# Kernel tuning notes

Hardware: AMD Instinct MI355X
Metric: run time of the kernel (lower is better)

## Reference

```python
import jax, jax.numpy as jnp
import numpy as np

B, S, D = 4, 2048, 1024  # batch, seq_len, input_dimension
KD, VD = 1024, 1024      # key_dim, value_dim


def setup_inputs() -> dict:
    key = jax.random.key(0)
    ks = jax.random.split(key, 9)
    sc_in = 1.0 / np.sqrt(D)
    sc_v = 1.0 / np.sqrt(VD)
    return {
        "x":  jax.random.normal(ks[0], (B, S, D), dtype=jnp.float32),
        "Wq": jax.random.normal(ks[1], (KD, D), dtype=jnp.float32) * sc_in,
        "bq": jax.random.normal(ks[2], (KD,), dtype=jnp.float32) * 0.01,
        "Wk": jax.random.normal(ks[3], (KD, D), dtype=jnp.float32) * sc_in,
        "bk": jax.random.normal(ks[4], (KD,), dtype=jnp.float32) * 0.01,
        "Wv": jax.random.normal(ks[5], (VD, D), dtype=jnp.float32) * sc_in,
        "bv": jax.random.normal(ks[6], (VD,), dtype=jnp.float32) * 0.01,
        "Wo": jax.random.normal(ks[7], (D, VD), dtype=jnp.float32) * sc_v,
        "bo": jax.random.normal(ks[8], (D,), dtype=jnp.float32) * 0.01,
    }


def reference(x, Wq, bq, Wk, bk, Wv, bv, Wo, bo):
    # projections (torch Linear: x @ W.T + b)
    q = jnp.einsum('bsd,kd->bsk', x, Wq) + bq   # (B,S,KD)
    k = jnp.einsum('bsd,kd->bsk', x, Wk) + bk   # (B,S,KD)
    v = jnp.einsum('bsd,vd->bsv', x, Wv) + bv   # (B,S,VD)

    scores = jnp.einsum('bqk,bsk->bqs', q, k) / jnp.sqrt(jnp.float32(KD))  # (B,S,S)

    # sign rescale: scores * sign(scores) (sign(0) mapped to 1) == |scores| with zeros kept
    sign_mask = jnp.sign(scores)
    sign_mask = sign_mask + (sign_mask == 0).astype(jnp.float32)

    # causal mask: lower-triangular (incl diag) multiplied by 1, strict upper -> -inf
    seq = scores.shape[-1]
    causal = jnp.tril(jnp.ones((seq, seq), dtype=bool))
    masked = jnp.where(causal, scores * sign_mask, -jnp.inf)

    weights = jax.nn.softmax(masked, axis=2)            # (B,S,S)
    out = jnp.einsum('bqs,bsv->bqv', weights, v)        # (B,S,VD)
    return jnp.einsum('bqv,dv->bqd', out, Wo) + bo      # (B,S,D)
```

## Files before the change

### kernel.cpp

```cpp
#include <hip/hip_runtime.h>
#include <hip/hip_bf16.h>
#include <cstdint>


#define BM 128

typedef __attribute__((ext_vector_type(8))) __bf16 bf16x8;
typedef __attribute__((ext_vector_type(4))) __bf16 bf16x4;
typedef __attribute__((ext_vector_type(4))) float floatx4;

__device__ __forceinline__ void async_copy16(const __bf16* g, const __bf16* l) {
  __builtin_amdgcn_global_load_lds(
      (const __attribute__((address_space(1))) unsigned int*)(const void*)g,
      (__attribute__((address_space(3))) unsigned int*)(unsigned)(uintptr_t)(const void*)l,
      16, 0, 0);
}

__device__ __forceinline__ void gemm_core(const __bf16* __restrict__ pA,
                                          const __bf16* __restrict__ pB,
                                          int K, int kBeg, int kEnd, int mb,
                                          int nb, floatx4 (&acc)[4][4]) {
  __shared__ __align__(16) __bf16 As0[BM * 32];
  __shared__ __align__(16) __bf16 As1[BM * 32];
  __shared__ __align__(16) __bf16 Bs0[BM * 32];
  __shared__ __align__(16) __bf16 Bs1[BM * 32];

  const int t = threadIdx.x;
  const int lane = t & 63;
  const int wave = t >> 6;
  const int quad = lane >> 4;
  const int l16 = lane & 15;
  const int wm = wave >> 1;
  const int wn = wave & 1;

  const __bf16* gA = pA + (long)(mb * BM + (t >> 2)) * K + ((t & 3) * 8);
  const __bf16* gB = pB + (long)(nb * BM + (t >> 2)) * K + ((t & 3) * 8);
  const long rowHalf = (long)64 * K;
  __bf16* lA0 = &As0[t * 8];
  __bf16* lA1 = &As1[t * 8];
  __bf16* lB0 = &Bs0[t * 8];
  __bf16* lB1 = &Bs1[t * 8];

  for (int kk = kBeg; kk < kEnd; ++kk) {
    const long ko = (long)kk * 64;
    async_copy16(gA + ko, lA0);
    async_copy16(gA + ko + rowHalf, lA0 + 2048);
    async_copy16(gA + ko + 32, lA1);
    async_copy16(gA + ko + 32 + rowHalf, lA1 + 2048);
    async_copy16(gB + ko, lB0);
    async_copy16(gB + ko + rowHalf, lB0 + 2048);
    async_copy16(gB + ko + 32, lB1);
    async_copy16(gB + ko + 32 + rowHalf, lB1 + 2048);
    __syncthreads();

#pragma unroll
    for (int p = 0; p < 2; ++p) {
      const __bf16* As = p ? As1 : As0;
      const __bf16* Bs = p ? Bs1 : Bs0;
      bf16x8 af[4], bfr[4];
#pragma unroll
      for (int i = 0; i < 4; ++i) {
        af[i] = *(const bf16x8*)&As[(wm * 64 + i * 16 + l16) * 32 + quad * 8];
        bfr[i] = *(const bf16x8*)&Bs[(wn * 64 + i * 16 + l16) * 32 + quad * 8];
      }
#pragma unroll
      for (int i = 0; i < 4; ++i)
#pragma unroll
        for (int j = 0; j < 4; ++j)
          acc[i][j] = __builtin_amdgcn_mfma_f32_16x16x32_bf16(af[i], bfr[j],
                                                              acc[i][j], 0, 0, 0);
    }
    __syncthreads();
  }
}

__device__ __forceinline__ float wave_sum(float s) {
  s += __shfl_xor(s, 1, 64);
  s += __shfl_xor(s, 2, 64);
  s += __shfl_xor(s, 4, 64);
  s += __shfl_xor(s, 8, 64);
  s += __shfl_xor(s, 16, 64);
  s += __shfl_xor(s, 32, 64);
  return s;
}

__global__ void __launch_bounds__(256, 2)
wcomb(const __bf16* __restrict__ Wqt, const __bf16* __restrict__ Wkt,
      const __bf16* __restrict__ Wob, const __bf16* __restrict__ Wvt,
      __bf16* __restrict__ Mqk, __bf16* __restrict__ Wvo,
      const float* __restrict__ bq, const float* __restrict__ bk,
      float* __restrict__ w1, float* __restrict__ w2, float* __restrict__ cbuf) {
  const int id = blockIdx.x;
  const int t = threadIdx.x;

  if (id < 128) {
    const bool isM = id < 64;
    const int wid = isM ? id : (id - 64);
    const int mb = wid >> 3, nb = wid & 7;
    const __bf16* pA = isM ? Wkt : Wob;
    const __bf16* pB = isM ? Wqt : Wvt;
    __bf16* C = isM ? Mqk : Wvo;

    floatx4 acc[4][4] = {};
    gemm_core(pA, pB, 1024, 0, 16, mb, nb, acc);

    const int lane = t & 63, wave = t >> 6;
    const int rb = (wave >> 1) * 64 + (lane >> 4) * 4;
    const int cb = (wave & 1) * 64 + (lane & 15);
#pragma unroll
    for (int j4 = 0; j4 < 4; ++j4) {
      const int gc = nb * 128 + cb + j4 * 16;
#pragma unroll
      for (int i = 0; i < 4; ++i) {
        const int gr = mb * BM + rb + i * 16;
#pragma unroll
        for (int r = 0; r < 4; ++r)
          C[(long)(gr + r) * 1024 + gc] = (__bf16)acc[i][j4][r];
      }
    }
  } else if (id < 144) {
    const bool is1 = id < 136;
    const int jb = is1 ? (id - 128) : (id - 136);
    const __bf16* Wt = is1 ? Wqt : Wkt;
    const float* bb = is1 ? bk : bq;
    float* ow = is1 ? w1 : w2;
    const int lane = t & 63, wave = t >> 6;
    for (int rr = 0; rr < 32; ++rr) {
      const int row = jb * 128 + wave * 32 + rr;
      const bf16x8 a0 = *(const bf16x8*)&Wt[(long)row * 1024 + lane * 16];
      const bf16x8 a1 = *(const bf16x8*)&Wt[(long)row * 1024 + lane * 16 + 8];
      float s = 0.f;
#pragma unroll
      for (int e = 0; e < 8; ++e) {
        s += (float)a0[e] * bb[lane * 16 + e];
        s += (float)a1[e] * bb[lane * 16 + 8 + e];
      }
      s = wave_sum(s);
      if (lane == 0) ow[row] = s;
    }
  } else {
    __shared__ float wsum[4];
    float s = 0.f;
    for (int i = t; i < 1024; i += 256) s += bq[i] * bk[i];
    s = wave_sum(s);
    if ((t & 63) == 0) wsum[t >> 6] = s;
    __syncthreads();
    if (t == 0) cbuf[0] = wsum[0] + wsum[1] + wsum[2] + wsum[3];
  }
}

__global__ void __launch_bounds__(256, 2)
proj(const __bf16* __restrict__ xb, const __bf16* __restrict__ Mqk,
     const __bf16* __restrict__ Wvo, const float* __restrict__ w2,
     const float* __restrict__ bvo, const float* __restrict__ w1,
     const float* __restrict__ cbuf, __bf16* __restrict__ yb,
     __bf16* __restrict__ Ut, float* __restrict__ r1, int S, int D) {
  const int id = blockIdx.x;
  const int t = threadIdx.x;

  if (id < 1024) {
    const bool isY = id < 512;
    const int pid = isY ? id : (id - 512);
    const int xcd = pid & 7;
    const int j = pid >> 3;
    const int mb = xcd * 8 + (j & 7);
    const int nb = j >> 3;
    const __bf16* pB = isY ? Mqk : Wvo;

    floatx4 acc[4][4] = {};
    gemm_core(xb, pB, D, 0, D / 64, mb, nb, acc);

    const int lane = t & 63, wave = t >> 6;
    const int rb = (wave >> 1) * 64 + (lane >> 4) * 4;
    const int cb = (wave & 1) * 64 + (lane & 15);

    if (isY) {
#pragma unroll
      for (int j4 = 0; j4 < 4; ++j4) {
        const int gc = nb * 128 + cb + j4 * 16;
        const float bv = w2[gc];
#pragma unroll
        for (int i = 0; i < 4; ++i) {
          const int gr = mb * BM + rb + i * 16;
#pragma unroll
          for (int r = 0; r < 4; ++r)
            yb[(long)(gr + r) * D + gc] = (__bf16)(acc[i][j4][r] + bv);
        }
      }
    } else {
      const int bb = (mb * BM) / S;
      const int s0 = mb * BM - bb * S;
#pragma unroll
      for (int j4 = 0; j4 < 4; ++j4) {
        const int gc = nb * 128 + cb + j4 * 16;
        const float bv = bvo[gc];
#pragma unroll
        for (int i = 0; i < 4; ++i) {
          const int sr = s0 + rb + i * 16;
          bf16x4 o;
#pragma unroll
          for (int r = 0; r < 4; ++r) o[r] = (__bf16)(acc[i][j4][r] + bv);
          *(bf16x4*)&Ut[((long)bb * D + gc) * S + sr] = o;
        }
      }
    }
  } else {
    const int jb = id - 1024;
    const float c = cbuf[0];
    const int lane = t & 63, wave = t >> 6;
    for (int rr = 0; rr < 32; ++rr) {
      const int row = jb * 128 + wave * 32 + rr;
      const bf16x8 a0 = *(const bf16x8*)&xb[(long)row * D + lane * 16];
      const bf16x8 a1 = *(const bf16x8*)&xb[(long)row * D + lane * 16 + 8];
      float s = 0.f;
#pragma unroll
      for (int e = 0; e < 8; ++e) {
        s += (float)a0[e] * w1[lane * 16 + e];
        s += (float)a1[e] * w1[lane * 16 + 8 + e];
      }
      s = wave_sum(s);
      if (lane == 0) r1[row] = s + c;
    }
  }
}

__global__ void __launch_bounds__(256, 2)
gemm_scores(const __bf16* __restrict__ yb, const __bf16* __restrict__ xb,
            const float* __restrict__ r1, __bf16* __restrict__ P,
            float* __restrict__ lsum, int S, int D) {
  const int id = blockIdx.x;
  const int xcd = id & 7;
  const int r = id >> 3;
  const int b = r / 17;
  const int ci = r - b * 17;
  const int n1 = xcd + 1;
  const int mb = (ci < n1) ? xcd : (15 - xcd);
  const int nb = (ci < n1) ? ci : (ci - n1);

  floatx4 acc[4][4] = {};
  gemm_core(yb + (long)b * S * D, xb + (long)b * S * D, D, 0, D / 64, mb, nb,
            acc);

  const int t = threadIdx.x;
  const int lane = t & 63, wave = t >> 6;
  const int l16 = lane & 15;
  const int rb = (wave >> 1) * 64 + (lane >> 4) * 4;
  const int cb = (wave & 1) * 64 + l16;
  __bf16* C = P + (long)b * S * S;
  float* lrow = lsum + (long)b * S;
  const float* r1b = r1 + (long)b * S;
  const float sc = 0.03125f;

#pragma unroll
  for (int i = 0; i < 4; ++i) {
#pragma unroll
    for (int r_ = 0; r_ < 4; ++r_) {
      const int row = mb * BM + rb + i * 16 + r_;
      const float rv = r1b[row];
      float psum = 0.f;
#pragma unroll
      for (int j4 = 0; j4 < 4; ++j4) {
        const int col = nb * 128 + cb + j4 * 16;
        const float p =
            (col <= row) ? __expf(fabsf((acc[i][j4][r_] + rv) * sc)) : 0.f;
        psum += p;
        C[(long)row * S + col] = (__bf16)p;
      }
      psum += __shfl_xor(psum, 1, 64);
      psum += __shfl_xor(psum, 2, 64);
      psum += __shfl_xor(psum, 4, 64);
      psum += __shfl_xor(psum, 8, 64);
      if (l16 == 0) atomicAdd(&lrow[row], psum);
    }
  }
}

__global__ void __launch_bounds__(256, 2)
gemm_pvo(const __bf16* __restrict__ P, const __bf16* __restrict__ Ut,
         const float* __restrict__ lsum, const float* __restrict__ bo,
         float* __restrict__ out, int S, int D) {
  const int id = blockIdx.x;
  const int xcd = id & 7;
  const int j = id >> 3;
  const int half = j >> 5;
  const int idx = j & 31;
  const int b = idx >> 3;
  const int nb = idx & 7;
  const int mb = half ? xcd : (15 - xcd);

  floatx4 acc[4][4] = {};
  gemm_core(P + (long)b * S * S, Ut + (long)b * D * S, S, 0, 2 * (mb + 1), mb,
            nb, acc);

  const int t = threadIdx.x;
  const int lane = t & 63, wave = t >> 6;
  const int rb = (wave >> 1) * 64 + (lane >> 4) * 4;
  const int cb = (wave & 1) * 64 + (lane & 15);
  const float* lrow = lsum + (long)b * S;

#pragma unroll
  for (int i = 0; i < 4; ++i) {
#pragma unroll
    for (int r_ = 0; r_ < 4; ++r_) {
      const int row = mb * BM + rb + i * 16 + r_;
      const float inv = 1.f / lrow[row];
#pragma unroll
      for (int j4 = 0; j4 < 4; ++j4) {
        const int col = nb * 128 + cb + j4 * 16;
        out[((long)b * S + row) * D + col] = acc[i][j4][r_] * inv + bo[col];
      }
    }
  }
}

__global__ void prep(const float* __restrict__ x, const float* __restrict__ Wq,
                     const float* __restrict__ Wk, const float* __restrict__ Wv,
                     const float* __restrict__ Wo, const float* __restrict__ bv,
                     __bf16* __restrict__ xb, __bf16* __restrict__ Wqt,
                     __bf16* __restrict__ Wkt, __bf16* __restrict__ Wvt,
                     __bf16* __restrict__ Wob, float* __restrict__ bvo,
                     float* __restrict__ lsum) {
  __shared__ __bf16 tile[64][66];
  __shared__ float wsum[4];
  const int bid = blockIdx.x;
  const int t = threadIdx.x;
  if (bid < 8192) {
    const long i = ((long)bid * 256 + t) * 4;
    const float4 f = *(const float4*)(x + i);
    bf16x4 o;
    o[0] = (__bf16)f.x; o[1] = (__bf16)f.y; o[2] = (__bf16)f.z; o[3] = (__bf16)f.w;
    *(bf16x4*)(xb + i) = o;
  } else if (bid < 8960) {
    const int which = (bid - 8192) >> 8;
    const int idx = (bid - 8192) & 255;
    const float* src = which == 0 ? Wq : (which == 1 ? Wk : Wv);
    __bf16* dst = which == 0 ? Wqt : (which == 1 ? Wkt : Wvt);
    const int r0 = (idx >> 4) * 64, c0 = (idx & 15) * 64;
#pragma unroll
    for (int e = 0; e < 16; ++e) {
      const int i = e * 256 + t;
      const int r = i >> 6, c = i & 63;
      tile[r][c] = (__bf16)src[(long)(r0 + r) * 1024 + (c0 + c)];
    }
    __syncthreads();
#pragma unroll
    for (int e = 0; e < 16; ++e) {
      const int i = e * 256 + t;
      const int r = i >> 6, c = i & 63;
      dst[(long)(c0 + r) * 1024 + (r0 + c)] = tile[c][r];
    }
  } else if (bid < 9984) {
    const long i = ((long)(bid - 8960) * 256 + t) * 4;
    const float4 f = *(const float4*)(Wo + i);
    bf16x4 o;
    o[0] = (__bf16)f.x; o[1] = (__bf16)f.y; o[2] = (__bf16)f.z; o[3] = (__bf16)f.w;
    *(bf16x4*)(Wob + i) = o;
  } else if (bid < 11008) {
    const int d = bid - 9984;
    const float* row = Wo + (long)d * 1024;
    float s = 0.f;
    for (int v = t; v < 1024; v += 256) s += bv[v] * row[v];
#pragma unroll
    for (int off = 32; off > 0; off >>= 1) s += __shfl_down(s, off, 64);
    if ((t & 63) == 0) wsum[t >> 6] = s;
    __syncthreads();
    if (t == 0) bvo[d] = wsum[0] + wsum[1] + wsum[2] + wsum[3];
  } else {
#pragma unroll
    for (int e = 0; e < 8; ++e)
      *(float4*)(lsum + (e * 256 + t) * 4) = float4{0.f, 0.f, 0.f, 0.f};
  }
}

extern "C" void kernel_launch(void* const* d_in, const int* in_sizes, int n_in,
                              void* d_out, int out_size, void* d_ws, size_t ws_size,
                              hipStream_t stream) {
  const float* x = (const float*)d_in[0];
  const float* Wq = (const float*)d_in[1];
  const float* bq = (const float*)d_in[2];
  const float* Wk = (const float*)d_in[3];
  const float* bk = (const float*)d_in[4];
  const float* Wv = (const float*)d_in[5];
  const float* bv = (const float*)d_in[6];
  const float* Wo = (const float*)d_in[7];
  const float* bo = (const float*)d_in[8];
  float* out = (float*)d_out;

  constexpr int B = 4, S = 2048, D = 1024;
  constexpr long MB_ = 1024 * 1024;

  char* w = (char*)d_ws;
  __bf16* xb  = (__bf16*)(w);
  __bf16* yb  = (__bf16*)(w + 16 * MB_);
  __bf16* Ut  = (__bf16*)(w + 32 * MB_);
  __bf16* P   = (__bf16*)(w + 48 * MB_);
  __bf16* Mqk = (__bf16*)(w + 80 * MB_);
  __bf16* Wvo = (__bf16*)(w + 82 * MB_);
  __bf16* Wqt = (__bf16*)(w + 84 * MB_);
  __bf16* Wkt = (__bf16*)(w + 86 * MB_);
  __bf16* Wvt = (__bf16*)(w + 88 * MB_);
  __bf16* Wob = (__bf16*)(w + 90 * MB_);
  float* lsum = (float*)(w + 92 * MB_);
  float* r1   = (float*)(w + 92 * MB_ + 32768);
  float* w1   = (float*)(w + 92 * MB_ + 65536);
  float* w2   = (float*)(w + 92 * MB_ + 69632);
  float* bvo  = (float*)(w + 92 * MB_ + 73728);
  float* cbuf = (float*)(w + 92 * MB_ + 77824);

  prep<<<11009, 256, 0, stream>>>(x, Wq, Wk, Wv, Wo, bv, xb, Wqt, Wkt, Wvt,
                                  Wob, bvo, lsum);

  wcomb<<<145, 256, 0, stream>>>(Wqt, Wkt, Wob, Wvt, Mqk, Wvo, bq, bk, w1, w2,
                                 cbuf);

  proj<<<1088, 256, 0, stream>>>(xb, Mqk, Wvo, w2, bvo, w1, cbuf, yb, Ut, r1,
                                 S, D);

  gemm_scores<<<544, 256, 0, stream>>>(yb, xb, r1, P, lsum, S, D);

  gemm_pvo<<<512, 256, 0, stream>>>(P, Ut, lsum, bo, out, S, D);
}
```

Before: 253.5 us.

## Fuse all five kernels into one persistent cooperative kernel with grid syncs

Replaces the five separate launches (prep, wcomb, proj, gemm_scores, gemm_pvo) with a single cooperative persistent kernel. Blocks loop over each stage's work items and a grid-wide sync separates the stages, all sharing one shared-memory buffer. The bias-projection reductions (w1, w2, bvo) are also rewritten to read the fp32 weights directly instead of the transposed bf16 copies. The aim is to cut launch gaps and tail effects between stages. In exchange it adds grid-sync cost, and the block-to-XCD mapping is no longer tied to blockIdx when the grid is smaller than the work count.

```diff
diff --git a/kernel.cpp b/kernel.cpp
--- a/kernel.cpp
+++ b/kernel.cpp
@@ -1,6 +1,9 @@
 #include <hip/hip_runtime.h>
+#include <hip/hip_cooperative_groups.h>
 #include <hip/hip_bf16.h>
 #include <cstdint>
+
+namespace cg = cooperative_groups;
 
 
 #define BM 128
@@ -8,6 +11,13 @@
 typedef __attribute__((ext_vector_type(8))) __bf16 bf16x8;
 typedef __attribute__((ext_vector_type(4))) __bf16 bf16x4;
 typedef __attribute__((ext_vector_type(4))) float floatx4;
+
+struct KArgs {
+  const float *x, *Wq, *bq, *Wk, *bk, *Wv, *bv, *Wo, *bo;
+  float* out;
+  __bf16 *xb, *yb, *Ut, *P, *Mqk, *Wvo, *Wqt, *Wkt, *Wvt, *Wob;
+  float *lsum, *r1, *w1, *w2, *bvo, *cbuf;
+};
 
 __device__ __forceinline__ void async_copy16(const __bf16* g, const __bf16* l) {
   __builtin_amdgcn_global_load_lds(
@@ -16,14 +26,14 @@
       16, 0, 0);
 }
 
-__device__ __forceinline__ void gemm_core(const __bf16* __restrict__ pA,
+__device__ __forceinline__ void gemm_core(__bf16* SM, const __bf16* __restrict__ pA,
                                           const __bf16* __restrict__ pB,
                                           int K, int kBeg, int kEnd, int mb,
                                           int nb, floatx4 (&acc)[4][4]) {
-  __shared__ __align__(16) __bf16 As0[BM * 32];
-  __shared__ __align__(16) __bf16 As1[BM * 32];
-  __shared__ __align__(16) __bf16 Bs0[BM * 32];
-  __shared__ __align__(16) __bf16 Bs1[BM * 32];
+  __bf16* As0 = SM;
+  __bf16* As1 = SM + 4096;
+  __bf16* Bs0 = SM + 8192;
+  __bf16* Bs1 = SM + 12288;
 
   const int t = threadIdx.x;
   const int lane = t & 63;
@@ -84,26 +94,102 @@
   return s;
 }
 
-__global__ void __launch_bounds__(256, 2)
-wcomb(const __bf16* __restrict__ Wqt, const __bf16* __restrict__ Wkt,
-      const __bf16* __restrict__ Wob, const __bf16* __restrict__ Wvt,
-      __bf16* __restrict__ Mqk, __bf16* __restrict__ Wvo,
-      const float* __restrict__ bq, const float* __restrict__ bk,
-      float* __restrict__ w1, float* __restrict__ w2, float* __restrict__ cbuf) {
-  const int id = blockIdx.x;
+__global__ void __launch_bounds__(256, 2) coop(KArgs a) {
+  __shared__ __align__(16) __bf16 SM[16384];
   const int t = threadIdx.x;
-
-  if (id < 128) {
-    const bool isM = id < 64;
-    const int wid = isM ? id : (id - 64);
+  const int gsz = gridDim.x;
+  cg::grid_group grid = cg::this_grid();
+  constexpr int S = 2048, D = 1024;
+
+  for (int bid = blockIdx.x; bid < 10010; bid += gsz) {
+    if (bid < 8192) {
+      const long i = ((long)bid * 256 + t) * 4;
+      const float4 f = *(const float4*)(a.x + i);
+      bf16x4 o;
+      o[0] = (__bf16)f.x; o[1] = (__bf16)f.y; o[2] = (__bf16)f.z; o[3] = (__bf16)f.w;
+      *(bf16x4*)(a.xb + i) = o;
+    } else if (bid < 8960) {
+      const int which = (bid - 8192) >> 8;
+      const int idx = (bid - 8192) & 255;
+      const float* src = which == 0 ? a.Wq : (which == 1 ? a.Wk : a.Wv);
+      __bf16* dst = which == 0 ? a.Wqt : (which == 1 ? a.Wkt : a.Wvt);
+      const int r0 = (idx >> 4) * 64, c0 = (idx & 15) * 64;
+      __bf16(*tile)[66] = reinterpret_cast<__bf16(*)[66]>(SM);
+      __syncthreads();
+#pragma unroll
+      for (int e = 0; e < 16; ++e) {
+        const int i = e * 256 + t;
+        const int r = i >> 6, c = i & 63;
+        tile[r][c] = (__bf16)src[(long)(r0 + r) * 1024 + (c0 + c)];
+      }
+      __syncthreads();
+#pragma unroll
+      for (int e = 0; e < 16; ++e) {
+        const int i = e * 256 + t;
+        const int r = i >> 6, c = i & 63;
+        dst[(long)(c0 + r) * 1024 + (r0 + c)] = tile[c][r];
+      }
+      __syncthreads();
+    } else if (bid < 9984) {
+      const long i = ((long)(bid - 8960) * 256 + t) * 4;
+      const float4 f = *(const float4*)(a.Wo + i);
+      bf16x4 o;
+      o[0] = (__bf16)f.x; o[1] = (__bf16)f.y; o[2] = (__bf16)f.z; o[3] = (__bf16)f.w;
+      *(bf16x4*)(a.Wob + i) = o;
+    } else if (bid < 9992) {
+      const int lane = t & 63, wave = t >> 6;
+      for (int rr = 0; rr < 32; ++rr) {
+        const int row = (bid - 9984) * 128 + wave * 32 + rr;
+        float s = 0.f;
+        for (int v = lane; v < 1024; v += 64) s += a.bv[v] * a.Wo[(long)row * 1024 + v];
+        s = wave_sum(s);
+        if (lane == 0) a.bvo[row] = s;
+      }
+    } else if (bid < 10008) {
+      const bool is1 = bid < 10000;
+      const int jb = is1 ? (bid - 9992) : (bid - 10000);
+      const float* W = is1 ? a.Wq : a.Wk;
+      const float* bb = is1 ? a.bk : a.bq;
+      float* ow = is1 ? a.w1 : a.w2;
+      const int d = jb * 128 + (t & 127);
+      const int half = t >> 7;
+      float s = 0.f;
+      for (int kd = half * 512; kd < half * 512 + 512; ++kd)
+        s += W[(long)kd * 1024 + d] * bb[kd];
+      float* fbuf = (float*)SM;
+      __syncthreads();
+      fbuf[t] = s;
+      __syncthreads();
+      if (t < 128) ow[jb * 128 + t] = fbuf[t] + fbuf[t + 128];
+      __syncthreads();
+    } else if (bid == 10008) {
+      float s = 0.f;
+      for (int i = t; i < 1024; i += 256) s += a.bq[i] * a.bk[i];
+      s = wave_sum(s);
+      float* fbuf = (float*)SM;
+      __syncthreads();
+      if ((t & 63) == 0) fbuf[t >> 6] = s;
+      __syncthreads();
+      if (t == 0) a.cbuf[0] = fbuf[0] + fbuf[1] + fbuf[2] + fbuf[3];
+      __syncthreads();
+    } else {
+#pragma unroll
+      for (int e = 0; e < 8; ++e)
+        *(float4*)(a.lsum + (e * 256 + t) * 4) = float4{0.f, 0.f, 0.f, 0.f};
+    }
+  }
+  __threadfence();
+  grid.sync();
+
+  for (int j = blockIdx.x; j < 128; j += gsz) {
+    const bool isM = j < 64;
+    const int wid = isM ? j : (j - 64);
     const int mb = wid >> 3, nb = wid & 7;
-    const __bf16* pA = isM ? Wkt : Wob;
-    const __bf16* pB = isM ? Wqt : Wvt;
-    __bf16* C = isM ? Mqk : Wvo;
-
+    const __bf16* pA = isM ? a.Wkt : a.Wob;
+    const __bf16* pB = isM ? a.Wqt : a.Wvt;
+    __bf16* C = isM ? a.Mqk : a.Wvo;
     floatx4 acc[4][4] = {};
-    gemm_core(pA, pB, 1024, 0, 16, mb, nb, acc);
-
+    gemm_core(SM, pA, pB, 1024, 0, 16, mb, nb, acc);
     const int lane = t & 63, wave = t >> 6;
     const int rb = (wave >> 1) * 64 + (lane >> 4) * 4;
     const int cb = (wave & 1) * 64 + (lane & 15);
@@ -118,305 +204,195 @@
           C[(long)(gr + r) * 1024 + gc] = (__bf16)acc[i][j4][r];
       }
     }
-  } else if (id < 144) {
-    const bool is1 = id < 136;
-    const int jb = is1 ? (id - 128) : (id - 136);
-    const __bf16* Wt = is1 ? Wqt : Wkt;
-    const float* bb = is1 ? bk : bq;
-    float* ow = is1 ? w1 : w2;
+  }
+  __threadfence();
+  grid.sync();
+
+  for (int j = blockIdx.x; j < 1088; j += gsz) {
+    if (j < 1024) {
+      const bool isY = j < 512;
+      const int pid = isY ? j : (j - 512);
+      const int xcd = pid & 7;
+      const int jj = pid >> 3;
+      const int mb = xcd * 8 + (jj & 7);
+      const int nb = jj >> 3;
+      const __bf16* pB = isY ? a.Mqk : a.Wvo;
+      floatx4 acc[4][4] = {};
+      gemm_core(SM, a.xb, pB, D, 0, D / 64, mb, nb, acc);
+      const int lane = t & 63, wave = t >> 6;
+      const int rb = (wave >> 1) * 64 + (lane >> 4) * 4;
+      const int cb = (wave & 1) * 64 + (lane & 15);
+      if (isY) {
+#pragma unroll
+        for (int j4 = 0; j4 < 4; ++j4) {
+          const int gc = nb * 128 + cb + j4 * 16;
+          const float bv = a.w2[gc];
+#pragma unroll
+          for (int i = 0; i < 4; ++i) {
+            const int gr = mb * BM + rb + i * 16;
+#pragma unroll
+            for (int r = 0; r < 4; ++r)
+              a.yb[(long)(gr + r) * D + gc] = (__bf16)(acc[i][j4][r] + bv);
+          }
+        }
+      } else {
+        const int bb = (mb * BM) / S;
+        const int s0 = mb * BM - bb * S;
+#pragma unroll
+        for (int j4 = 0; j4 < 4; ++j4) {
+          const int gc = nb * 128 + cb + j4 * 16;
+          const float bv = a.bvo[gc];
+#pragma unroll
+          for (int i = 0; i < 4; ++i) {
+            const int sr = s0 + rb + i * 16;
+            bf16x4 o;
+#pragma unroll
+            for (int r = 0; r < 4; ++r) o[r] = (__bf16)(acc[i][j4][r] + bv);
+            *(bf16x4*)&a.Ut[((long)bb * D + gc) * S + sr] = o;
+          }
+        }
+      }
+    } else {
+      const int jb = j - 1024;
+      const float c = a.cbuf[0];
+      const int lane = t & 63, wave = t >> 6;
+      for (int rr = 0; rr < 32; ++rr) {
+        const int row = jb * 128 + wave * 32 + rr;
+        const bf16x8 a0 = *(const bf16x8*)&a.xb[(long)row * D + lane * 16];
+        const bf16x8 a1 = *(const bf16x8*)&a.xb[(long)row * D + lane * 16 + 8];
+        float s = 0.f;
+#pragma unroll
+        for (int e = 0; e < 8; ++e) {
+          s += (float)a0[e] * a.w1[lane * 16 + e];
+          s += (float)a1[e] * a.w1[lane * 16 + 8 + e];
+        }
+        s = wave_sum(s);
+        if (lane == 0) a.r1[row] = s + c;
+      }
+    }
+  }
+  __threadfence();
+  grid.sync();
+
+  for (int j = blockIdx.x; j < 544; j += gsz) {
+    const int xcd = j & 7;
+    const int r = j >> 3;
+    const int b = r / 17;
+    const int ci = r - b * 17;
+    const int n1 = xcd + 1;
+    const int mb = (ci < n1) ? xcd : (15 - xcd);
+    const int nb = (ci < n1) ? ci : (ci - n1);
+    floatx4 acc[4][4] = {};
+    gemm_core(SM, a.yb + (long)b * S * D, a.xb + (long)b * S * D, D, 0, D / 64,
+              mb, nb, acc);
     const int lane = t & 63, wave = t >> 6;
-    for (int rr = 0; rr < 32; ++rr) {
-      const int row = jb * 128 + wave * 32 + rr;
-      const bf16x8 a0 = *(const bf16x8*)&Wt[(long)row * 1024 + lane * 16];
-      const bf16x8 a1 = *(const bf16x8*)&Wt[(long)row * 1024 + lane * 16 + 8];
-      float s = 0.f;
-#pragma unroll
-      for (int e = 0; e < 8; ++e) {
-        s += (float)a0[e] * bb[lane * 16 + e];
-        s += (float)a1[e] * bb[lane * 16 + 8 + e];
-      }
-      s = wave_sum(s);
-      if (lane == 0) ow[row] = s;
-    }
-  } else {
-    __shared__ float wsum[4];
-    float s = 0.f;
-    for (int i = t; i < 1024; i += 256) s += bq[i] * bk[i];
-    s = wave_sum(s);
-    if ((t & 63) == 0) wsum[t >> 6] = s;
-    __syncthreads();
-    if (t == 0) cbuf[0] = wsum[0] + wsum[1] + wsum[2] + wsum[3];
-  }
-}
-
-__global__ void __launch_bounds__(256, 2)
-proj(const __bf16* __restrict__ xb, const __bf16* __restrict__ Mqk,
-     const __bf16* __restrict__ Wvo, const float* __restrict__ w2,
-     const float* __restrict__ bvo, const float* __restrict__ w1,
-     const float* __restrict__ cbuf, __bf16* __restrict__ yb,
-     __bf16* __restrict__ Ut, float* __restrict__ r1, int S, int D) {
-  const int id = blockIdx.x;
-  const int t = threadIdx.x;
-
-  if (id < 1024) {
-    const bool isY = id < 512;
-    const int pid = isY ? id : (id - 512);
-    const int xcd = pid & 7;
-    const int j = pid >> 3;
-    const int mb = xcd * 8 + (j & 7);
-    const int nb = j >> 3;
-    const __bf16* pB = isY ? Mqk : Wvo;
-
+    const int l16 = lane & 15;
+    const int rb = (wave >> 1) * 64 + (lane >> 4) * 4;
+    const int cb = (wave & 1) * 64 + l16;
+    __bf16* C = a.P + (long)b * S * S;
+    float* lrow = a.lsum + (long)b * S;
+    const float* r1b = a.r1 + (long)b * S;
+    const float sc = 0.03125f;
+#pragma unroll
+    for (int i = 0; i < 4; ++i) {
+#pragma unroll
+      for (int r_ = 0; r_ < 4; ++r_) {
+        const int row = mb * BM + rb + i * 16 + r_;
+        const float rv = r1b[row];
+        float psum = 0.f;
+#pragma unroll
+        for (int j4 = 0; j4 < 4; ++j4) {
+          const int col = nb * 128 + cb + j4 * 16;
+          const float p =
+              (col <= row) ? __expf(fabsf((acc[i][j4][r_] + rv) * sc)) : 0.f;
+          psum += p;
+          C[(long)row * S + col] = (__bf16)p;
+        }
+        psum += __shfl_xor(psum, 1, 64);
+        psum += __shfl_xor(psum, 2, 64);
+        psum += __shfl_xor(psum, 4, 64);
+        psum += __shfl_xor(psum, 8, 64);
+        if (l16 == 0) atomicAdd(&lrow[row], psum);
+      }
+    }
+  }
+  __threadfence();
+  grid.sync();
+
+  for (int j = blockIdx.x; j < 512; j += gsz) {
+    const int xcd = j & 7;
+    const int jj = j >> 3;
+    const int half = jj >> 5;
+    const int idx = jj & 31;
+    const int b = idx >> 3;
+    const int nb = idx & 7;
+    const int mb = half ? xcd : (15 - xcd);
     floatx4 acc[4][4] = {};
-    gemm_core(xb, pB, D, 0, D / 64, mb, nb, acc);
-
+    gemm_core(SM, a.P + (long)b * S * S, a.Ut + (long)b * D * S, S, 0,
+              2 * (mb + 1), mb, nb, acc);
     const int lane = t & 63, wave = t >> 6;
     const int rb = (wave >> 1) * 64 + (lane >> 4) * 4;
     const int cb = (wave & 1) * 64 + (lane & 15);
-
-    if (isY) {
-#pragma unroll
-      for (int j4 = 0; j4 < 4; ++j4) {
-        const int gc = nb * 128 + cb + j4 * 16;
-        const float bv = w2[gc];
-#pragma unroll
-        for (int i = 0; i < 4; ++i) {
-          const int gr = mb * BM + rb + i * 16;
-#pragma unroll
-          for (int r = 0; r < 4; ++r)
-            yb[(long)(gr + r) * D + gc] = (__bf16)(acc[i][j4][r] + bv);
-        }
-      }
-    } else {
-      const int bb = (mb * BM) / S;
-      const int s0 = mb * BM - bb * S;
-#pragma unroll
-      for (int j4 = 0; j4 < 4; ++j4) {
-        const int gc = nb * 128 + cb + j4 * 16;
-        const float bv = bvo[gc];
-#pragma unroll
-        for (int i = 0; i < 4; ++i) {
-          const int sr = s0 + rb + i * 16;
-          bf16x4 o;
-#pragma unroll
-          for (int r = 0; r < 4; ++r) o[r] = (__bf16)(acc[i][j4][r] + bv);
-          *(bf16x4*)&Ut[((long)bb * D + gc) * S + sr] = o;
-        }
-      }
-    }
-  } else {
-    const int jb = id - 1024;
-    const float c = cbuf[0];
-    const int lane = t & 63, wave = t >> 6;
-    for (int rr = 0; rr < 32; ++rr) {
-      const int row = jb * 128 + wave * 32 + rr;
-      const bf16x8 a0 = *(const bf16x8*)&xb[(long)row * D + lane * 16];
-      const bf16x8 a1 = *(const bf16x8*)&xb[(long)row * D + lane * 16 + 8];
-      float s = 0.f;
-#pragma unroll
-      for (int e = 0; e < 8; ++e) {
-        s += (float)a0[e] * w1[lane * 16 + e];
-        s += (float)a1[e] * w1[lane * 16 + 8 + e];
-      }
-      s = wave_sum(s);
-      if (lane == 0) r1[row] = s + c;
-    }
-  }
-}
-
-__global__ void __launch_bounds__(256, 2)
-gemm_scores(const __bf16* __restrict__ yb, const __bf16* __restrict__ xb,
-            const float* __restrict__ r1, __bf16* __restrict__ P,
-            float* __restrict__ lsum, int S, int D) {
-  const int id = blockIdx.x;
-  const int xcd = id & 7;
-  const int r = id >> 3;
-  const int b = r / 17;
-  const int ci = r - b * 17;
-  const int n1 = xcd + 1;
-  const int mb = (ci < n1) ? xcd : (15 - xcd);
-  const int nb = (ci < n1) ? ci : (ci - n1);
-
-  floatx4 acc[4][4] = {};
-  gemm_core(yb + (long)b * S * D, xb + (long)b * S * D, D, 0, D / 64, mb, nb,
-            acc);
-
-  const int t = threadIdx.x;
-  const int lane = t & 63, wave = t >> 6;
-  const int l16 = lane & 15;
-  const int rb = (wave >> 1) * 64 + (lane >> 4) * 4;
-  const int cb = (wave & 1) * 64 + l16;
-  __bf16* C = P + (long)b * S * S;
-  float* lrow = lsum + (long)b * S;
-  const float* r1b = r1 + (long)b * S;
-  const float sc = 0.03125f;
-
-#pragma unroll
-  for (int i = 0; i < 4; ++i) {
-#pragma unroll
-    for (int r_ = 0; r_ < 4; ++r_) {
-      const int row = mb * BM + rb + i * 16 + r_;
-      const float rv = r1b[row];
-      float psum = 0.f;
-#pragma unroll
-      for (int j4 = 0; j4 < 4; ++j4) {
-        const int col = nb * 128 + cb + j4 * 16;
-        const float p =
-            (col <= row) ? __expf(fabsf((acc[i][j4][r_] + rv) * sc)) : 0.f;
-        psum += p;
-        C[(long)row * S + col] = (__bf16)p;
-      }
-      psum += __shfl_xor(psum, 1, 64);
-      psum += __shfl_xor(psum, 2, 64);
-      psum += __shfl_xor(psum, 4, 64);
-      psum += __shfl_xor(psum, 8, 64);
-      if (l16 == 0) atomicAdd(&lrow[row], psum);
-    }
-  }
-}
-
-__global__ void __launch_bounds__(256, 2)
-gemm_pvo(const __bf16* __restrict__ P, const __bf16* __restrict__ Ut,
-         const float* __restrict__ lsum, const float* __restrict__ bo,
-         float* __restrict__ out, int S, int D) {
-  const int id = blockIdx.x;
-  const int xcd = id & 7;
-  const int j = id >> 3;
-  const int half = j >> 5;
-  const int idx = j & 31;
-  const int b = idx >> 3;
-  const int nb = idx & 7;
-  const int mb = half ? xcd : (15 - xcd);
-
-  floatx4 acc[4][4] = {};
-  gemm_core(P + (long)b * S * S, Ut + (long)b * D * S, S, 0, 2 * (mb + 1), mb,
-            nb, acc);
-
-  const int t = threadIdx.x;
-  const int lane = t & 63, wave = t >> 6;
-  const int rb = (wave >> 1) * 64 + (lane >> 4) * 4;
-  const int cb = (wave & 1) * 64 + (lane & 15);
-  const float* lrow = lsum + (long)b * S;
-
-#pragma unroll
-  for (int i = 0; i < 4; ++i) {
-#pragma unroll
-    for (int r_ = 0; r_ < 4; ++r_) {
-      const int row = mb * BM + rb + i * 16 + r_;
-      const float inv = 1.f / lrow[row];
-#pragma unroll
-      for (int j4 = 0; j4 < 4; ++j4) {
-        const int col = nb * 128 + cb + j4 * 16;
-        out[((long)b * S + row) * D + col] = acc[i][j4][r_] * inv + bo[col];
-      }
-    }
-  }
-}
-
-__global__ void prep(const float* __restrict__ x, const float* __restrict__ Wq,
-                     const float* __restrict__ Wk, const float* __restrict__ Wv,
-                     const float* __restrict__ Wo, const float* __restrict__ bv,
-                     __bf16* __restrict__ xb, __bf16* __restrict__ Wqt,
-                     __bf16* __restrict__ Wkt, __bf16* __restrict__ Wvt,
-                     __bf16* __restrict__ Wob, float* __restrict__ bvo,
-                     float* __restrict__ lsum) {
-  __shared__ __bf16 tile[64][66];
-  __shared__ float wsum[4];
-  const int bid = blockIdx.x;
-  const int t = threadIdx.x;
-  if (bid < 8192) {
-    const long i = ((long)bid * 256 + t) * 4;
-    const float4 f = *(const float4*)(x + i);
-    bf16x4 o;
-    o[0] = (__bf16)f.x; o[1] = (__bf16)f.y; o[2] = (__bf16)f.z; o[3] = (__bf16)f.w;
-    *(bf16x4*)(xb + i) = o;
-  } else if (bid < 8960) {
-    const int which = (bid - 8192) >> 8;
-    const int idx = (bid - 8192) & 255;
-    const float* src = which == 0 ? Wq : (which == 1 ? Wk : Wv);
-    __bf16* dst = which == 0 ? Wqt : (which == 1 ? Wkt : Wvt);
-    const int r0 = (idx >> 4) * 64, c0 = (idx & 15) * 64;
-#pragma unroll
-    for (int e = 0; e < 16; ++e) {
-      const int i = e * 256 + t;
-      const int r = i >> 6, c = i & 63;
-      tile[r][c] = (__bf16)src[(long)(r0 + r) * 1024 + (c0 + c)];
-    }
-    __syncthreads();
-#pragma unroll
-    for (int e = 0; e < 16; ++e) {
-      const int i = e * 256 + t;
-      const int r = i >> 6, c = i & 63;
-      dst[(long)(c0 + r) * 1024 + (r0 + c)] = tile[c][r];
-    }
-  } else if (bid < 9984) {
-    const long i = ((long)(bid - 8960) * 256 + t) * 4;
-    const float4 f = *(const float4*)(Wo + i);
-    bf16x4 o;
-    o[0] = (__bf16)f.x; o[1] = (__bf16)f.y; o[2] = (__bf16)f.z; o[3] = (__bf16)f.w;
-    *(bf16x4*)(Wob + i) = o;
-  } else if (bid < 11008) {
-    const int d = bid - 9984;
-    const float* row = Wo + (long)d * 1024;
-    float s = 0.f;
-    for (int v = t; v < 1024; v += 256) s += bv[v] * row[v];
-#pragma unroll
-    for (int off = 32; off > 0; off >>= 1) s += __shfl_down(s, off, 64);
-    if ((t & 63) == 0) wsum[t >> 6] = s;
-    __syncthreads();
-    if (t == 0) bvo[d] = wsum[0] + wsum[1] + wsum[2] + wsum[3];
-  } else {
-#pragma unroll
-    for (int e = 0; e < 8; ++e)
-      *(float4*)(lsum + (e * 256 + t) * 4) = float4{0.f, 0.f, 0.f, 0.f};
+    const float* lrow = a.lsum + (long)b * S;
+#pragma unroll
+    for (int i = 0; i < 4; ++i) {
+#pragma unroll
+      for (int r_ = 0; r_ < 4; ++r_) {
+        const int row = mb * BM + rb + i * 16 + r_;
+        const float inv = 1.f / lrow[row];
+#pragma unroll
+        for (int j4 = 0; j4 < 4; ++j4) {
+          const int col = nb * 128 + cb + j4 * 16;
+          a.out[((long)b * S + row) * D + col] = acc[i][j4][r_] * inv + a.bo[col];
+        }
+      }
+    }
   }
 }
 
 extern "C" void kernel_launch(void* const* d_in, const int* in_sizes, int n_in,
                               void* d_out, int out_size, void* d_ws, size_t ws_size,
                               hipStream_t stream) {
-  const float* x = (const float*)d_in[0];
-  const float* Wq = (const float*)d_in[1];
-  const float* bq = (const float*)d_in[2];
-  const float* Wk = (const float*)d_in[3];
-  const float* bk = (const float*)d_in[4];
-  const float* Wv = (const float*)d_in[5];
-  const float* bv = (const float*)d_in[6];
-  const float* Wo = (const float*)d_in[7];
-  const float* bo = (const float*)d_in[8];
-  float* out = (float*)d_out;
-
-  constexpr int B = 4, S = 2048, D = 1024;
   constexpr long MB_ = 1024 * 1024;
-
   char* w = (char*)d_ws;
-  __bf16* xb  = (__bf16*)(w);
-  __bf16* yb  = (__bf16*)(w + 16 * MB_);
-  __bf16* Ut  = (__bf16*)(w + 32 * MB_);
-  __bf16* P   = (__bf16*)(w + 48 * MB_);
-  __bf16* Mqk = (__bf16*)(w + 80 * MB_);
-  __bf16* Wvo = (__bf16*)(w + 82 * MB_);
-  __bf16* Wqt = (__bf16*)(w + 84 * MB_);
-  __bf16* Wkt = (__bf16*)(w + 86 * MB_);
-  __bf16* Wvt = (__bf16*)(w + 88 * MB_);
-  __bf16* Wob = (__bf16*)(w + 90 * MB_);
-  float* lsum = (float*)(w + 92 * MB_);
-  float* r1   = (float*)(w + 92 * MB_ + 32768);
-  float* w1   = (float*)(w + 92 * MB_ + 65536);
-  float* w2   = (float*)(w + 92 * MB_ + 69632);
-  float* bvo  = (float*)(w + 92 * MB_ + 73728);
-  float* cbuf = (float*)(w + 92 * MB_ + 77824);
-
-  prep<<<11009, 256, 0, stream>>>(x, Wq, Wk, Wv, Wo, bv, xb, Wqt, Wkt, Wvt,
-                                  Wob, bvo, lsum);
-
-  wcomb<<<145, 256, 0, stream>>>(Wqt, Wkt, Wob, Wvt, Mqk, Wvo, bq, bk, w1, w2,
-                                 cbuf);
-
-  proj<<<1088, 256, 0, stream>>>(xb, Mqk, Wvo, w2, bvo, w1, cbuf, yb, Ut, r1,
-                                 S, D);
-
-  gemm_scores<<<544, 256, 0, stream>>>(yb, xb, r1, P, lsum, S, D);
-
-  gemm_pvo<<<512, 256, 0, stream>>>(P, Ut, lsum, bo, out, S, D);
-}
+
+  KArgs ka;
+  ka.x = (const float*)d_in[0];
+  ka.Wq = (const float*)d_in[1];
+  ka.bq = (const float*)d_in[2];
+  ka.Wk = (const float*)d_in[3];
+  ka.bk = (const float*)d_in[4];
+  ka.Wv = (const float*)d_in[5];
+  ka.bv = (const float*)d_in[6];
+  ka.Wo = (const float*)d_in[7];
+  ka.bo = (const float*)d_in[8];
+  ka.out = (float*)d_out;
+  ka.xb = (__bf16*)(w);
+  ka.yb = (__bf16*)(w + 16 * MB_);
+  ka.Ut = (__bf16*)(w + 32 * MB_);
+  ka.P = (__bf16*)(w + 48 * MB_);
+  ka.Mqk = (__bf16*)(w + 80 * MB_);
+  ka.Wvo = (__bf16*)(w + 82 * MB_);
+  ka.Wqt = (__bf16*)(w + 84 * MB_);
+  ka.Wkt = (__bf16*)(w + 86 * MB_);
+  ka.Wvt = (__bf16*)(w + 88 * MB_);
+  ka.Wob = (__bf16*)(w + 90 * MB_);
+  ka.lsum = (float*)(w + 92 * MB_);
+  ka.r1 = (float*)(w + 92 * MB_ + 32768);
+  ka.w1 = (float*)(w + 92 * MB_ + 65536);
+  ka.w2 = (float*)(w + 92 * MB_ + 69632);
+  ka.bvo = (float*)(w + 92 * MB_ + 73728);
+  ka.cbuf = (float*)(w + 92 * MB_ + 77824);
+
+  int occ = 0;
+  (void)hipOccupancyMaxActiveBlocksPerMultiprocessor(&occ, coop, 256, 0);
+  if (occ < 1) occ = 1;
+  long grid = (long)occ * 256;
+  if (grid > 1024) grid = 1024;
+  grid &= ~7L;
+  if (grid < 8) grid = 8;
+
+  void* args[] = {(void*)&ka};
+  (void)hipLaunchCooperativeKernel(coop, dim3((unsigned)grid), dim3(256), args,
+                                   0, stream);
+}
```

Result: slower. 706.7 us (+178.8%).
